# Optimization experiments

Measured on AMD Instinct MI355X. Metric: run time of the kernel, lower is better.

Reference implementation:

```python
import jax, jax.numpy as jnp
import numpy as np

N_NODES = 100000
N_EDGES = 3200000
NUM_FEATURES = 128
NH = 64
NUM_CLASSES = 32
K = 6
K_MIX = 2
W_SCALE = 0.05


def setup_inputs() -> dict:
    key = jax.random.key(0)
    ks = jax.random.split(key, 16)
    inp = {
        "x": jax.random.normal(ks[0], (N_NODES, NUM_FEATURES), jnp.float32),
        "edge_index": jax.random.randint(ks[1], (2, N_EDGES), 0, N_NODES, jnp.int32),
        "W0": jax.random.normal(ks[2], (K, NUM_FEATURES, NH), jnp.float32) * W_SCALE,
        "b0": jnp.zeros((NH,), jnp.float32),
        "Ws0": jax.random.normal(ks[3], (1, NUM_FEATURES, NH), jnp.float32) * W_SCALE,
        "bs0": jnp.zeros((NH,), jnp.float32),
        "W1": jax.random.normal(ks[4], (K, NH, NH), jnp.float32) * W_SCALE,
        "b1": jnp.zeros((NH,), jnp.float32),
        "Ws1": jax.random.normal(ks[5], (1, NH, NH), jnp.float32) * W_SCALE,
        "bs1": jnp.zeros((NH,), jnp.float32),
        "W2": jax.random.normal(ks[6], (K, NH, NH), jnp.float32) * W_SCALE,
        "b2": jnp.zeros((NH,), jnp.float32),
        "Ws2": jax.random.normal(ks[7], (1, NH, NH), jnp.float32) * W_SCALE,
        "bs2": jnp.zeros((NH,), jnp.float32),
        "Wmix": jax.random.normal(ks[8], (K_MIX, NH + NUM_FEATURES, NUM_CLASSES), jnp.float32) * W_SCALE,
        "bmix": jnp.zeros((NUM_CLASSES,), jnp.float32),
    }
    return inp


def _cheb_conv(h, src, dst, norm_w, Wk, b, n_nodes):
    # Chebyshev recursion with L_hat = -D^{-1/2} A D^{-1/2} (lambda_max = 2,
    # sym normalization -> self-loop terms of the scaled Laplacian cancel).
    def prop(t):  # L_hat @ t : one sparse hop (gather -> scale -> scatter-add)
        return -jax.ops.segment_sum(norm_w[:, None] * t[src], dst, num_segments=n_nodes)

    k_hops = Wk.shape[0]
    Tx0 = h
    out = Tx0 @ Wk[0]
    if k_hops > 1:
        Tx1 = prop(Tx0)
        out = out + Tx1 @ Wk[1]
        for k in range(2, k_hops):
            Tx2 = 2.0 * prop(Tx1) - Tx0
            out = out + Tx2 @ Wk[k]
            Tx0, Tx1 = Tx1, Tx2
    return out + b


def reference(x, edge_index, W0, b0, Ws0, bs0, W1, b1, Ws1, bs1,
              W2, b2, Ws2, bs2, Wmix, bmix):
    n = x.shape[0]
    src, dst = edge_index[0], edge_index[1]
    deg = jax.ops.segment_sum(jnp.ones_like(src, jnp.float32), dst, num_segments=n)
    dis = jnp.where(deg > 0, jax.lax.rsqrt(jnp.maximum(deg, 1.0)), 0.0)
    norm_w = dis[src] * dis[dst]  # per-edge sym-normalized weight

    h = x
    for (W, b, Ws, bs) in ((W0, b0, Ws0, bs0), (W1, b1, Ws1, bs1), (W2, b2, Ws2, bs2)):
        # Kipfblock (relu, dropout is identity in eval mode) + K=1 skip ChebConv
        h = jax.nn.relu(_cheb_conv(h, src, dst, norm_w, W, b, n)) \
            + _cheb_conv(h, src, dst, norm_w, Ws, bs, n)
    h = jnp.concatenate((h, x), axis=1)  # in/out skip connection
    return _cheb_conv(h, src, dst, norm_w, Wmix, bmix, n)
```

## Files before the change

kernel.cpp:

```cpp
#include <hip/hip_runtime.h>
#include <hip/hip_bf16.h>
#include <cstdio>
#include <cstdint>

typedef __hip_bfloat16 bf16;
typedef __attribute__((ext_vector_type(8)))  short short8v;
typedef __attribute__((ext_vector_type(4)))  float f32x4;

static __device__ __forceinline__ float b2f(bf16 v){ return __bfloat162float(v); }
static __device__ __forceinline__ bf16  f2b(float v){ return __float2bfloat16(v); }
static __device__ __forceinline__ float ldf(const float* p){ return *p; }
static __device__ __forceinline__ float ldf(const bf16* p){ return b2f(*p); }

static __device__ __forceinline__ float bl(uint32_t u){ union{uint32_t i; float f;} c; c.i = u<<16;          return c.f; }
static __device__ __forceinline__ float bh(uint32_t u){ union{uint32_t i; float f;} c; c.i = u & 0xffff0000u; return c.f; }
static __device__ __forceinline__ uint32_t pk(float lo, float hi){
  bf16 a=f2b(lo), b=f2b(hi);
  uint16_t ai=*reinterpret_cast<uint16_t*>(&a), bi=*reinterpret_cast<uint16_t*>(&b);
  return ((uint32_t)bi<<16) | ai;
}
static __device__ __forceinline__ void ld2(const bf16* p, unsigned i32, float& lo, float& hi){
  uint32_t u = reinterpret_cast<const uint32_t*>(p)[i32]; lo=bl(u); hi=bh(u);
}
static __device__ __forceinline__ void ld2(const float* p, unsigned i32, float& lo, float& hi){
  float2 v = reinterpret_cast<const float2*>(p)[i32]; lo=v.x; hi=v.y;
}
static __device__ __forceinline__ void st2(bf16* p, unsigned i32, float lo, float hi){
  reinterpret_cast<uint32_t*>(p)[i32] = pk(lo,hi);
}
static __device__ __forceinline__ void st2(float* p, unsigned i32, float lo, float hi){
  reinterpret_cast<float2*>(p)[i32] = make_float2(lo,hi);
}


__global__ void k_count(const int* __restrict__ dst, int* __restrict__ deg, int E){
  int e = blockIdx.x*256 + threadIdx.x;
  if(e<E) atomicAdd(&deg[dst[e]], 1);
}

__global__ void k_scan1(const int* __restrict__ deg, int* __restrict__ rp1, int* __restrict__ bsums, int N){
  __shared__ int s[256];
  int i = blockIdx.x*256 + threadIdx.x;
  int v = (i<N)? deg[i] : 0;
  s[threadIdx.x]=v; __syncthreads();
  for(int off=1; off<256; off<<=1){
    int t = (threadIdx.x>=off)? s[threadIdx.x-off] : 0;
    __syncthreads();
    s[threadIdx.x]+=t;
    __syncthreads();
  }
  if(i<N) rp1[i]=s[threadIdx.x];
  if(threadIdx.x==255) bsums[blockIdx.x]=s[255];
}

__global__ void k_scan2(const int* __restrict__ bsums, int* __restrict__ boffs, int NB){
  __shared__ int s[512];
  int x=threadIdx.x;
  int v = (x<NB)? bsums[x] : 0;
  s[x]=v; __syncthreads();
  for(int off=1; off<512; off<<=1){
    int t=(x>=off)? s[x-off]:0; __syncthreads();
    s[x]+=t; __syncthreads();
  }
  if(x<NB) boffs[x]=s[x]-v;
}

__global__ void k_scan3(int* __restrict__ row_ptr, const int* __restrict__ boffs,
                        const int* __restrict__ deg, float* __restrict__ dis, float* __restrict__ dinv, int N){
  int i = blockIdx.x*256+threadIdx.x;
  if(i<N){
    row_ptr[i+1] += boffs[blockIdx.x];
    int d = deg[i];
    dis[i]  = (d>0)? rsqrtf((float)d) : 0.f;
    dinv[i] = (d>0)? sqrtf((float)d)  : 0.f;
    if(i==0) row_ptr[0]=0;
  }
}

__global__ void k_fill(const int* __restrict__ src, const int* __restrict__ dst,
                       const int* __restrict__ row_ptr, int* __restrict__ deg,
                       int* __restrict__ csr_src, int E){
  int e = blockIdx.x*256+threadIdx.x;
  if(e<E){
    int d = dst[e];
    int pos = row_ptr[d] + atomicAdd(&deg[d],-1) - 1;
    csr_src[pos] = src[e];
  }
}

__global__ void k_prep(const float* __restrict__ W0, const float* __restrict__ Ws0,
                       const float* __restrict__ W1, const float* __restrict__ Ws1,
                       const float* __restrict__ W2, const float* __restrict__ Ws2,
                       const float* __restrict__ Wmix,
                       bf16* __restrict__ WT0, bf16* __restrict__ WT1,
                       bf16* __restrict__ WT2, bf16* __restrict__ WTm){
  int idx = blockIdx.x*256 + threadIdx.x;
  if(idx < 57344){
    int w = idx >> 13, r = idx & 8191;
    int k = r >> 6, n = r & 63;
    float v = (w==0)? Ws0[(k<<6)+n] : W0[(((6-w)<<7) + k)*64 + n];
    WT0[(size_t)((w<<6)+n)*136 + k] = f2b(v);
  } else if(idx < 57344+28672){
    int i2 = idx - 57344;
    int w = i2 >> 12, r = i2 & 4095;
    int k = r >> 6, n = r & 63;
    float v = (w==0)? Ws1[(k<<6)+n] : W1[(((6-w)<<6) + k)*64 + n];
    WT1[(size_t)((w<<6)+n)*72 + k] = f2b(v);
  } else if(idx < 57344+2*28672){
    int i2 = idx - (57344+28672);
    int w = i2 >> 12, r = i2 & 4095;
    int k = r >> 6, n = r & 63;
    float v = (w==0)? Ws2[(k<<6)+n] : W2[(((6-w)<<6) + k)*64 + n];
    WT2[(size_t)((w<<6)+n)*72 + k] = f2b(v);
  } else if(idx < 57344+2*28672+12288){
    int i2 = idx - (57344+2*28672);
    int n = i2 / 192, k = i2 % 192;
    float v = (n<32)? Wmix[k*32 + n] : Wmix[6144 + k*32 + (n-32)];
    WTm[(size_t)n*200 + k] = f2b(v);
  }
}

template<int K, int NW, int AMODE>
__global__ __launch_bounds__(256,2) void k_mfma(
    const bf16* __restrict__ Ab, const float* __restrict__ Af, const bf16* __restrict__ WT,
    bf16* __restrict__ O0, bf16* __restrict__ O1, bf16* __restrict__ O2, bf16* __restrict__ O3,
    bf16* __restrict__ O4, bf16* __restrict__ O5, bf16* __restrict__ O6,
    float* __restrict__ Zf, const float* __restrict__ dis, int M)
{
  constexpr int Kp = K + 8;
  static_assert(Kp % 8 == 0, "Kp must keep 16B alignment");
  constexpr int NS = K / 32;
  constexpr int NSLOT = (NW>1) ? 2 : 1;
  __shared__ short sA[128][Kp];
  __shared__ short sW[NSLOT][64][Kp];

  const int t    = threadIdx.x;
  const int m0   = blockIdx.x * 128;
  const int l    = t & 63;
  const int wid  = t >> 6;
  const int wrow = (wid >> 1) * 64;
  const int wcol = (wid & 1) * 32;
  const int l4   = l & 15;
  const int lk8  = (l >> 4) * 8;

  bf16* const Ol[7] = {O0,O1,O2,O3,O4,O5,O6};
  const short8v szero = {0,0,0,0,0,0,0,0};
  const f32x4   fzero = {0.f,0.f,0.f,0.f};

  constexpr int WCH = (64*Kp)/8;
  constexpr int WIT = (WCH + 255)/256;
  short8v wreg[WIT];
  auto loadW = [&](int w){
    #pragma unroll
    for(int it=0; it<WIT; ++it){
      int c = t + it*256;
      if(c < WCH) wreg[it] = *reinterpret_cast<const short8v*>(&WT[(size_t)w*(64*Kp) + (size_t)c*8]);
    }
  };
  auto writeW = [&](int slot){
    short* base = &sW[slot][0][0];
    #pragma unroll
    for(int it=0; it<WIT; ++it){
      int c = t + it*256;
      if(c < WCH) *reinterpret_cast<short8v*>(base + (size_t)c*8) = wreg[it];
    }
  };

  loadW(0);

  {
    constexpr int CPR = K/8;
    #pragma unroll
    for(int it=0; it<(128*CPR)/256; ++it){
      int c = t + it*256;
      int row = c / CPR, j = c % CPR;
      int m = m0 + row;
      short8v v = szero;
      if(m < M){
        if constexpr(AMODE==0){
          v = *reinterpret_cast<const short8v*>(&Ab[(size_t)m*K + j*8]);
        } else if constexpr(AMODE==1){
          float4 f0 = *reinterpret_cast<const float4*>(&Af[(size_t)m*K + j*8]);
          float4 f1 = *reinterpret_cast<const float4*>(&Af[(size_t)m*K + j*8 + 4]);
          bf16* hp = reinterpret_cast<bf16*>(&v);
          hp[0]=f2b(f0.x); hp[1]=f2b(f0.y); hp[2]=f2b(f0.z); hp[3]=f2b(f0.w);
          hp[4]=f2b(f1.x); hp[5]=f2b(f1.y); hp[6]=f2b(f1.z); hp[7]=f2b(f1.w);
        } else {
          if(j < 8){
            v = *reinterpret_cast<const short8v*>(&Ab[(size_t)m*64 + j*8]);
          } else {
            float4 f0 = *reinterpret_cast<const float4*>(&Af[(size_t)m*128 + (j-8)*8]);
            float4 f1 = *reinterpret_cast<const float4*>(&Af[(size_t)m*128 + (j-8)*8 + 4]);
            bf16* hp = reinterpret_cast<bf16*>(&v);
            hp[0]=f2b(f0.x); hp[1]=f2b(f0.y); hp[2]=f2b(f0.z); hp[3]=f2b(f0.w);
            hp[4]=f2b(f1.x); hp[5]=f2b(f1.y); hp[6]=f2b(f1.z); hp[7]=f2b(f1.w);
          }
        }
      }
      *reinterpret_cast<short8v*>(&sA[row][j*8]) = v;
    }
  }

  writeW(0);
  __syncthreads();

  short8v af[4][(NS>0)?NS:1];
  if constexpr(NW > 1){
    #pragma unroll
    for(int rt=0; rt<4; ++rt)
      #pragma unroll
      for(int s=0; s<NS; ++s)
        af[rt][s] = *reinterpret_cast<const short8v*>(&sA[wrow + rt*16 + l4][s*32 + lk8]);
  }

  #pragma unroll
  for(int w=0; w<NW; ++w){
    if(w+1 < NW) loadW(w+1);

    f32x4 acc[4][2];
    #pragma unroll
    for(int rt=0; rt<4; ++rt){ acc[rt][0]=fzero; acc[rt][1]=fzero; }

    const short* wb = &sW[(NW>1)?(w&1):0][0][0];
    #pragma unroll
    for(int s=0; s<NS; ++s){
      short8v b0 = *reinterpret_cast<const short8v*>(wb + (size_t)(wcol +      l4)*Kp + s*32 + lk8);
      short8v b1 = *reinterpret_cast<const short8v*>(wb + (size_t)(wcol + 16 + l4)*Kp + s*32 + lk8);
      #pragma unroll
      for(int rt=0; rt<4; ++rt){
        short8v a = (NW>1) ? af[rt][s]
                  : *reinterpret_cast<const short8v*>(&sA[wrow + rt*16 + l4][s*32 + lk8]);
        acc[rt][0] = __builtin_amdgcn_mfma_f32_16x16x32_bf16(a, b0, acc[rt][0], 0,0,0);
        acc[rt][1] = __builtin_amdgcn_mfma_f32_16x16x32_bf16(a, b1, acc[rt][1], 0,0,0);
      }
    }

    if(w+1 < NW){ writeW((w+1)&1); __syncthreads(); }

    #pragma unroll
    for(int rt=0; rt<4; ++rt){
      #pragma unroll
      for(int r=0; r<4; ++r){
        int row = m0 + wrow + rt*16 + ((l>>4)<<2) + r;
        if(row < M){
          if constexpr(AMODE != 2){
            float sc = 1.f;
            if(NW>1 && w==1) sc = dis[row];
            #pragma unroll
            for(int ct=0; ct<2; ++ct){
              float vv = acc[rt][ct][r] * sc;
              Ol[w][(size_t)row*64 + wcol + ct*16 + l4] = f2b(vv);
            }
          } else {
            float dm = dis[row];
            #pragma unroll
            for(int ct=0; ct<2; ++ct){
              int col = wcol + ct*16 + l4;
              float vv = acc[rt][ct][r];
              if(col < 32) Zf[(size_t)row*32 + col] = vv;
              else         O0[(size_t)row*32 + (col-32)] = f2b(vv*dm);
            }
          }
        }
      }
    }
  }
}

template<int F, int MODE, typename ZT, typename OT>
__global__ __launch_bounds__(256) void k_prop(const int* __restrict__ row_ptr, const int* __restrict__ csr_src,
    const float* __restrict__ dis, const float* __restrict__ dinv, const bf16* __restrict__ BinS,
    const ZT* __restrict__ Z, const bf16* __restrict__ BsubS,
    const float* __restrict__ bias, const bf16* __restrict__ Zs, const float* __restrict__ bias2,
    OT* __restrict__ out, int N){
  constexpr int L   = F/2;
  constexpr int NPB = 256/L;
  int v = blockIdx.x*NPB + threadIdx.x/L;
  if(v>=N) return;
  int f2 = threadIdx.x % L;
  const uint32_t* __restrict__ B32 = reinterpret_cast<const uint32_t*>(BinS);
  int e0=row_ptr[v], e1=row_ptr[v+1];
  unsigned idx32 = (unsigned)v*L + f2;

  float zL, zH; ld2(Z, idx32, zL, zH);
  float bsL=0.f, bsH=0.f;
  if constexpr(MODE==1 || MODE==2){
    uint32_t bu = reinterpret_cast<const uint32_t*>(BsubS)[idx32]; bsL=bl(bu); bsH=bh(bu);
  }
  float biL=0.f, biH=0.f;
  if constexpr(MODE>=2){
    float2 bv = reinterpret_cast<const float2*>(bias)[f2]; biL=bv.x; biH=bv.y;
  }
  float zsL=0.f, zsH=0.f, b2L=0.f, b2H=0.f;
  if constexpr(MODE==2){
    uint32_t su = reinterpret_cast<const uint32_t*>(Zs)[idx32]; zsL=bl(su); zsH=bh(su);
    float2 b2v = reinterpret_cast<const float2*>(bias2)[f2]; b2L=b2v.x; b2H=b2v.y;
  }
  float dv = dis[v];
  float di = dinv[v];

  float aL=0.f, aH=0.f;
  int e=e0;
  for(; e+L<=e1; e+=L){
    int si = csr_src[e + f2];
    #pragma unroll
    for(int c=0; c<L/16; ++c){
      int s[16];
      #pragma unroll
      for(int j=0;j<16;++j) s[j] = __shfl(si, c*16+j, L);
      uint32_t u[16];
      #pragma unroll
      for(int j=0;j<16;++j) u[j]=B32[(unsigned)s[j]*L + f2];
      #pragma unroll
      for(int j=0;j<16;++j){ aL+=bl(u[j]); aH+=bh(u[j]); }
    }
  }
  if(e+16<=e1){
    int s[16];
    #pragma unroll
    for(int j=0;j<16;++j) s[j]=csr_src[e+j];
    uint32_t u[16];
    #pragma unroll
    for(int j=0;j<16;++j) u[j]=B32[(unsigned)s[j]*L + f2];
    #pragma unroll
    for(int j=0;j<16;++j){ aL+=bl(u[j]); aH+=bh(u[j]); }
    e+=16;
  }
  if(e+8<=e1){
    int s[8];
    #pragma unroll
    for(int j=0;j<8;++j) s[j]=csr_src[e+j];
    uint32_t u[8];
    #pragma unroll
    for(int j=0;j<8;++j) u[j]=B32[(unsigned)s[j]*L + f2];
    #pragma unroll
    for(int j=0;j<8;++j){ aL+=bl(u[j]); aH+=bh(u[j]); }
    e+=8;
  }
  if(e<e1){
    #pragma unroll
    for(int j=0;j<8;++j){
      int idx=e+j;
      int s=csr_src[idx<e1 ? idx : e0];
      uint32_t uu=B32[(unsigned)s*L + f2];
      if(idx<e1){ aL+=bl(uu); aH+=bh(uu); }
    }
  }
  aL*=dv; aH*=dv;
  float rL, rH;
  if constexpr(MODE==0){ rL = zL - 2.f*aL;              rH = zH - 2.f*aH; }
  else if constexpr(MODE==1){ rL = zL - 2.f*aL - bsL*di; rH = zH - 2.f*aH - bsH*di; }
  else if constexpr(MODE==2){
    float tL = zL - aL - bsL*di + biL;
    float tH = zH - aH - bsH*di + biH;
    rL = fmaxf(tL,0.f) + zsL + b2L;
    rH = fmaxf(tH,0.f) + zsH + b2H;
  } else { rL = zL - aL + biL; rH = zH - aH + biH; }
  if constexpr(MODE<=1) st2(out, idx32, dv*rL, dv*rH);
  else                  st2(out, idx32, rL, rH);
}


extern "C" void kernel_launch(void* const* d_in, const int* in_sizes, int n_in,
                              void* d_out, int out_size, void* d_ws, size_t ws_size,
                              hipStream_t stream) {
  const int N = in_sizes[0]/128;
  const int E = in_sizes[1]/2;

  const float* x    = (const float*)d_in[0];
  const int*   ei   = (const int*  )d_in[1];
  const float* W0   = (const float*)d_in[2];
  const float* b0   = (const float*)d_in[3];
  const float* Ws0  = (const float*)d_in[4];
  const float* bs0  = (const float*)d_in[5];
  const float* W1   = (const float*)d_in[6];
  const float* b1   = (const float*)d_in[7];
  const float* Ws1  = (const float*)d_in[8];
  const float* bs1  = (const float*)d_in[9];
  const float* W2   = (const float*)d_in[10];
  const float* b2   = (const float*)d_in[11];
  const float* Ws2  = (const float*)d_in[12];
  const float* bs2  = (const float*)d_in[13];
  const float* Wmix = (const float*)d_in[14];
  const float* bmix = (const float*)d_in[15];
  float* out = (float*)d_out;

  const int* src = ei;
  const int* dst = ei + E;

  size_t off=0;
  char* ws=(char*)d_ws;
  auto alloc=[&](size_t bytes)->void*{ void* p = ws+off; off=(off+bytes+255)&~(size_t)255; return p; };
  int*   csr_src = (int*)  alloc((size_t)E*4);
  int*   row_ptr = (int*)  alloc((size_t)(N+1)*4);
  int*   deg     = (int*)  alloc((size_t)N*4);
  float* dis     = (float*)alloc((size_t)N*4);
  float* dinv    = (float*)alloc((size_t)N*4);
  int*   bsums   = (int*)  alloc(2048);
  int*   boffs   = (int*)  alloc(2048);
  bf16*  Z0      = (bf16*) alloc((size_t)N*64*2);
  bf16*  Z1      = (bf16*) alloc((size_t)N*64*2);
  bf16*  Z2      = (bf16*) alloc((size_t)N*64*2);
  bf16*  Z3      = (bf16*) alloc((size_t)N*64*2);
  bf16*  Z4      = (bf16*) alloc((size_t)N*64*2);
  bf16*  Zsb     = (bf16*) alloc((size_t)N*64*2);
  bf16*  P0s     = (bf16*) alloc((size_t)N*64*2);
  bf16*  P1s     = (bf16*) alloc((size_t)N*64*2);
  bf16*  P2s     = (bf16*) alloc((size_t)N*64*2);
  bf16*  hA      = (bf16*) alloc((size_t)N*64*2);
  bf16*  hB      = (bf16*) alloc((size_t)N*64*2);
  bf16*  WT0     = (bf16*) alloc((size_t)7*64*136*2);
  bf16*  WT1     = (bf16*) alloc((size_t)7*64*72*2);
  bf16*  WT2     = (bf16*) alloc((size_t)7*64*72*2);
  bf16*  WTm     = (bf16*) alloc((size_t)64*200*2);
  if(off > ws_size){
    fprintf(stderr, "kernel_launch: workspace too small: need %zu, have %zu\n", off, ws_size);
    return;
  }

  const int NB   = (N+255)/256;
  const int gE   = (E+255)/256;
  const int gM   = (N+127)/128;
  const int gP64 = (N+7)/8;
  const int gP32 = (N+15)/16;

  k_prep<<<496,256,0,stream>>>(W0,Ws0,W1,Ws1,W2,Ws2,Wmix, WT0,WT1,WT2,WTm);

  hipMemsetAsync(deg, 0, (size_t)N*4, stream);
  k_count<<<gE,256,0,stream>>>(dst, deg, E);
  k_scan1<<<NB,256,0,stream>>>(deg, row_ptr+1, bsums, N);
  k_scan2<<<1,512,0,stream>>>(bsums, boffs, NB);
  k_scan3<<<NB,256,0,stream>>>(row_ptr, boffs, deg, dis, dinv, N);
  k_fill<<<gE,256,0,stream>>>(src, dst, row_ptr, deg, csr_src, E);

  auto PROPS=[&](const float* b, const float* bs_, bf16* hout){
    k_prop<64,0,bf16,bf16><<<gP64,256,0,stream>>>(row_ptr,csr_src,dis,dinv,P0s,Z4,nullptr,nullptr,nullptr,nullptr,P1s,N);
    k_prop<64,1,bf16,bf16><<<gP64,256,0,stream>>>(row_ptr,csr_src,dis,dinv,P1s,Z3,P0s,nullptr,nullptr,nullptr,P2s,N);
    k_prop<64,1,bf16,bf16><<<gP64,256,0,stream>>>(row_ptr,csr_src,dis,dinv,P2s,Z2,P1s,nullptr,nullptr,nullptr,P0s,N);
    k_prop<64,1,bf16,bf16><<<gP64,256,0,stream>>>(row_ptr,csr_src,dis,dinv,P0s,Z1,P2s,nullptr,nullptr,nullptr,P1s,N);
    k_prop<64,2,bf16,bf16><<<gP64,256,0,stream>>>(row_ptr,csr_src,dis,dinv,P1s,Z0,P0s,b,Zsb,bs_,hout,N);
  };

  k_mfma<128,7,1><<<gM,256,0,stream>>>(nullptr, x, WT0, Zsb,P0s,Z4,Z3,Z2,Z1,Z0, nullptr, dis, N);
  PROPS(b0, bs0, hA);
  k_mfma<64,7,0><<<gM,256,0,stream>>>(hA, nullptr, WT1, Zsb,P0s,Z4,Z3,Z2,Z1,Z0, nullptr, dis, N);
  PROPS(b1, bs1, hB);
  k_mfma<64,7,0><<<gM,256,0,stream>>>(hB, nullptr, WT2, Zsb,P0s,Z4,Z3,Z2,Z1,Z0, nullptr, dis, N);
  PROPS(b2, bs2, hA);

  float* Zmixf = (float*)Z1;
  k_mfma<192,1,2><<<gM,256,0,stream>>>(hA, x, WTm, P0s,nullptr,nullptr,nullptr,nullptr,nullptr,nullptr, Zmixf, dis, N);
  k_prop<32,3,float,float><<<gP32,256,0,stream>>>(row_ptr,csr_src,dis,dinv,P0s,Zmixf,nullptr,bmix,nullptr,nullptr,out,N);
}
```

Before: 1.538 ms.

## Bucket edges by destination block before CSR fill for locality

```diff
diff --git a/kernel.cpp b/kernel.cpp
--- a/kernel.cpp
+++ b/kernel.cpp
@@ -85,6 +85,66 @@
     int d = dst[e];
     int pos = row_ptr[d] + atomicAdd(&deg[d],-1) - 1;
     csr_src[pos] = src[e];
+  }
+}
+
+
+__global__ void k_hist(const int* __restrict__ dst, int* __restrict__ chunk_hist,
+                       int* __restrict__ btot, int E, int nbuk, int epc){
+  __shared__ int h[1600];
+  for(int i=threadIdx.x;i<nbuk;i+=256) h[i]=0;
+  __syncthreads();
+  int base=blockIdx.x*epc, end=min(base+epc,E);
+  for(int e=base+(int)threadIdx.x; e<end; e+=256) atomicAdd(&h[dst[e]>>6],1);
+  __syncthreads();
+  for(int i=threadIdx.x;i<nbuk;i+=256){
+    int hv=h[i];
+    chunk_hist[(size_t)i*256 + blockIdx.x]=hv;
+    if(hv) atomicAdd(&btot[i],hv);
+  }
+}
+
+__global__ void k_bfix(const int* __restrict__ binc, const int* __restrict__ btot,
+                       const int* __restrict__ boffs, int* __restrict__ bbase, int nbuk){
+  int i=blockIdx.x*256+threadIdx.x;
+  if(i<nbuk) bbase[i] = binc[i] + boffs[i>>8] - btot[i];
+}
+
+__global__ void k_cscan(int* __restrict__ chunk_hist, const int* __restrict__ bbase, int nbuk){
+  __shared__ int s[256];
+  int b=blockIdx.x; if(b>=nbuk) return;
+  int x=threadIdx.x;
+  int v=chunk_hist[(size_t)b*256+x];
+  s[x]=v; __syncthreads();
+  for(int off=1; off<256; off<<=1){
+    int t=(x>=off)? s[x-off]:0; __syncthreads();
+    s[x]+=t; __syncthreads();
+  }
+  chunk_hist[(size_t)b*256+x] = s[x]-v + bbase[b];
+}
+
+__global__ void k_bscat(const int* __restrict__ src, const int* __restrict__ dst,
+                        const int* __restrict__ cbase, uint2* __restrict__ ebuf,
+                        int E, int nbuk, int epc){
+  __shared__ int cur[1600];
+  for(int i=threadIdx.x;i<nbuk;i+=256) cur[i]=cbase[(size_t)i*256 + blockIdx.x];
+  __syncthreads();
+  int base=blockIdx.x*epc, end=min(base+epc,E);
+  for(int e=base+(int)threadIdx.x; e<end; e+=256){
+    int d=dst[e], s=src[e];
+    int p=atomicAdd(&cur[d>>6],1);
+    ebuf[p]=make_uint2((unsigned)s,(unsigned)d);
+  }
+}
+
+__global__ void k_fill2(const uint2* __restrict__ ebuf, const int* __restrict__ row_ptr,
+                        int* __restrict__ deg, int* __restrict__ csr_src, int E){
+  int e = blockIdx.x*256+threadIdx.x;
+  if(e<E){
+    uint2 p = ebuf[e];
+    int d=(int)p.y;
+    int pos = row_ptr[d] + atomicAdd(&deg[d],-1) - 1;
+    csr_src[pos] = (int)p.x;
   }
 }
 
@@ -424,14 +484,38 @@
   const int gP64 = (N+7)/8;
   const int gP32 = (N+15)/16;
 
+  const int nbuk = (N+63)>>6;
+  const int NB2  = (nbuk+255)/256;
+  const int epc  = (E+255)/256;
+  const bool fast_fill = (nbuk <= 1600);
+  char*  gs         = (char*)Z0;
+  uint2* ebuf       = (uint2*)gs;
+  int*   chunk_hist = (int*)(gs + (((size_t)E*8 + 255) & ~(size_t)255));
+  int*   binc       = chunk_hist + (size_t)nbuk*256;
+  int*   btot       = binc + nbuk;
+  int*   bbase      = btot + nbuk;
+
   k_prep<<<496,256,0,stream>>>(W0,Ws0,W1,Ws1,W2,Ws2,Wmix, WT0,WT1,WT2,WTm);
 
   hipMemsetAsync(deg, 0, (size_t)N*4, stream);
   k_count<<<gE,256,0,stream>>>(dst, deg, E);
+  if(fast_fill){
+    hipMemsetAsync(btot, 0, (size_t)nbuk*4, stream);
+    k_hist<<<256,256,0,stream>>>(dst, chunk_hist, btot, E, nbuk, epc);
+    k_scan1<<<NB2,256,0,stream>>>(btot, binc, bsums, nbuk);
+    k_scan2<<<1,512,0,stream>>>(bsums, boffs, NB2);
+    k_bfix<<<NB2,256,0,stream>>>(binc, btot, boffs, bbase, nbuk);
+    k_cscan<<<nbuk,256,0,stream>>>(chunk_hist, bbase, nbuk);
+  }
   k_scan1<<<NB,256,0,stream>>>(deg, row_ptr+1, bsums, N);
   k_scan2<<<1,512,0,stream>>>(bsums, boffs, NB);
   k_scan3<<<NB,256,0,stream>>>(row_ptr, boffs, deg, dis, dinv, N);
-  k_fill<<<gE,256,0,stream>>>(src, dst, row_ptr, deg, csr_src, E);
+  if(fast_fill){
+    k_bscat<<<256,256,0,stream>>>(src, dst, chunk_hist, ebuf, E, nbuk, epc);
+    k_fill2<<<gE,256,0,stream>>>(ebuf, row_ptr, deg, csr_src, E);
+  } else {
+    k_fill<<<gE,256,0,stream>>>(src, dst, row_ptr, deg, csr_src, E);
+  }
 
   auto PROPS=[&](const float* b, const float* bs_, bf16* hout){
     k_prop<64,0,bf16,bf16><<<gP64,256,0,stream>>>(row_ptr,csr_src,dis,dinv,P0s,Z4,nullptr,nullptr,nullptr,nullptr,P1s,N);
```

Measured after the change: 1.596 ms. 3.8% more time.
